# Performance work log

Hardware: AMD Instinct MI355X
Metric: run time of the kernel (lower is better)

The kernel has to match this reference:

```python
import jax, jax.numpy as jnp
import numpy as np

D = 4096  # uniform layer width (sizes[i])
L = 4     # number of MyLinear layers (maximum)


def setup_inputs() -> dict:
    key = jax.random.key(0)
    ks = jax.random.split(key, 8)
    x = jax.random.normal(ks[0], (D,), jnp.float32)
    W_in = jax.random.normal(ks[1], (D, D), jnp.float32) / np.float32(np.sqrt(D))
    b_in = jax.random.normal(ks[2], (D,), jnp.float32) * 0.01
    weights = jax.random.normal(ks[3], (L, D, D), jnp.float32) / np.float32(np.sqrt(D))
    # `order` is a fixed 0/1-style connectivity mask (requires_grad=False in torch)
    orders = (jax.random.uniform(ks[4], (L, D, D)) < 0.5).astype(jnp.float32)
    biases = jax.random.normal(ks[5], (L, D), jnp.float32) * 0.01
    # input_layer[i]: which node slots feed layer i (irregular gather)
    gather_idx = jax.random.randint(ks[6], (L, D), 0, D)
    # layer_nodes[k]: where layer outputs are scattered (per-layer permutation)
    scatter_idx = jnp.stack(
        [jax.random.permutation(jax.random.fold_in(ks[7], i), D) for i in range(L + 1)]
    )
    return dict(x=x, W_in=W_in, b_in=b_in, weights=weights, orders=orders,
                biases=biases, gather_idx=gather_idx, scatter_idx=scatter_idx)


def reference(x, W_in, b_in, weights, orders, biases, gather_idx, scatter_idx):
    # input layer: relu(Linear(x)), scattered into the node buffer
    out0 = jax.nn.relu(W_in @ x + b_in)              # [D]
    buf = jnp.zeros_like(out0).at[scatter_idx[0]].set(out0)

    def step(buf, layer):
        W, O, b, g, s = layer
        inp = buf[g]                                  # gather node values [D]
        out = jax.nn.relu((W * O) @ inp + b)          # masked GEMV + bias + relu
        new_buf = jnp.zeros_like(out).at[s].set(out)  # scatter into node buffer
        return new_buf, out

    _, outs = jax.lax.scan(
        step, buf, (weights, orders, biases, gather_idx, scatter_idx[1:])
    )
    return outs[-1]  # forward returns the last layer's (pre-scatter) output
```

## Files before the change

kernel.cpp:

```cpp
#include <hip/hip_runtime.h>
#include <hip/hip_bf16.h>


#define DD 4096
#define NB 256
#define NT 1024
#define NLAYER 4

__device__ __forceinline__ void grid_barrier(int* cnt) {
    __syncthreads();
    if (threadIdx.x == 0) {
        __threadfence();
        __hip_atomic_fetch_add(cnt, 1, __ATOMIC_ACQ_REL, __HIP_MEMORY_SCOPE_AGENT);
        while (__hip_atomic_load(cnt, __ATOMIC_ACQUIRE, __HIP_MEMORY_SCOPE_AGENT) < NB) {}
        __threadfence();
    }
    __syncthreads();
}

__global__ __launch_bounds__(NT, 4)
void fused_net(const float* __restrict__ x,
               const float* __restrict__ W_in,
               const float* __restrict__ b_in,
               const float* __restrict__ weights,
               const float* __restrict__ orders,
               const float* __restrict__ biases,
               const int*   __restrict__ gidx,
               const int*   __restrict__ sidx,
               float*       __restrict__ out,
               float*       __restrict__ buf0,
               float*       __restrict__ buf1,
               int*         __restrict__ cnt)
{
    __shared__ float sh[DD];
    const int tid  = threadIdx.x;
    const int lane = tid & 63;
    const int wv   = tid >> 6;
    const int row  = blockIdx.x * 16 + wv;

    for (int j = tid; j < DD; j += NT) sh[j] = x[j];
    __syncthreads();
    {
        const float* Wr = W_in + (size_t)row * DD + lane * 4;
        float a0 = 0.f, a1 = 0.f, a2 = 0.f, a3 = 0.f;
        #pragma unroll
        for (int it = 0; it < 16; ++it) {
            float4 w = *reinterpret_cast<const float4*>(Wr + it * 256);
            float4 v = *reinterpret_cast<const float4*>(sh + it * 256 + lane * 4);
            a0 = fmaf(w.x, v.x, a0); a1 = fmaf(w.y, v.y, a1);
            a2 = fmaf(w.z, v.z, a2); a3 = fmaf(w.w, v.w, a3);
        }
        float acc = (a0 + a1) + (a2 + a3);
        #pragma unroll
        for (int off = 32; off; off >>= 1) acc += __shfl_xor(acc, off, 64);
        if (lane == 0) buf0[sidx[row]] = fmaxf(acc + b_in[row], 0.f);
    }
    grid_barrier(cnt + 0);

    float* bufs[2] = { buf0, buf1 };
    #pragma unroll
    for (int l = 0; l < NLAYER; ++l) {
        const float* src = bufs[l & 1];
        const int*   g   = gidx + (size_t)l * DD;
        for (int j = tid; j < DD; j += NT) sh[j] = src[g[j]];
        __syncthreads();

        const float* Wr = weights + (size_t)l * DD * DD + (size_t)row * DD + lane * 4;
        const float* Or = orders  + (size_t)l * DD * DD + (size_t)row * DD + lane * 4;
        float a0 = 0.f, a1 = 0.f, a2 = 0.f, a3 = 0.f;
        #pragma unroll
        for (int it = 0; it < 16; ++it) {
            float4 w = *reinterpret_cast<const float4*>(Wr + it * 256);
            float4 o = *reinterpret_cast<const float4*>(Or + it * 256);
            float4 v = *reinterpret_cast<const float4*>(sh + it * 256 + lane * 4);
            a0 = fmaf(w.x * o.x, v.x, a0);
            a1 = fmaf(w.y * o.y, v.y, a1);
            a2 = fmaf(w.z * o.z, v.z, a2);
            a3 = fmaf(w.w * o.w, v.w, a3);
        }
        float acc = (a0 + a1) + (a2 + a3);
        #pragma unroll
        for (int off = 32; off; off >>= 1) acc += __shfl_xor(acc, off, 64);
        float r = fmaxf(acc + biases[(size_t)l * DD + row], 0.f);

        if (l == NLAYER - 1) {
            if (lane == 0) out[row] = r;
        } else {
            if (lane == 0) bufs[(l + 1) & 1][sidx[(size_t)(l + 1) * DD + row]] = r;
            grid_barrier(cnt + 1 + l);
        }
    }
}

extern "C" void kernel_launch(void* const* d_in, const int* in_sizes, int n_in,
                              void* d_out, int out_size, void* d_ws, size_t ws_size,
                              hipStream_t stream) {
    const float* x       = (const float*)d_in[0];
    const float* W_in    = (const float*)d_in[1];
    const float* b_in    = (const float*)d_in[2];
    const float* weights = (const float*)d_in[3];
    const float* orders  = (const float*)d_in[4];
    const float* biases  = (const float*)d_in[5];
    const int*   gidx    = (const int*)d_in[6];
    const int*   sidx    = (const int*)d_in[7];
    float*       out     = (float*)d_out;

    int*   cnt  = (int*)d_ws;
    float* buf0 = (float*)((char*)d_ws + 256);
    float* buf1 = buf0 + DD;

    hipMemsetAsync(d_ws, 0, 256, stream);

    fused_net<<<NB, NT, 0, stream>>>(x, W_in, b_in, weights, orders, biases,
                                     gidx, sidx, out, buf0, buf1, cnt);
}
```

Baseline: 660.4 us.

## Split each row across two waves and double the grid to 512 blocks

Each block now handles 8 rows, with two wavefronts each computing half of a row's dot product. The halves are combined through shared memory, so the grid doubles to 512 blocks and launch bounds rise to 8. The inner loop software-prefetches the next weight and mask float4, and the barrier spin adds s_sleep to reduce atomic polling pressure. The aim is more memory-level parallelism across CUs for this bandwidth-bound masked GEMV. The cost is an extra shared-memory reduction and more blocks arriving at each grid barrier, and the persistent-grid scheme now relies on all 512 blocks being co-resident.

```diff
diff --git a/kernel.cpp b/kernel.cpp
--- a/kernel.cpp
+++ b/kernel.cpp
@@ -3,22 +3,58 @@
 
 
 #define DD 4096
-#define NB 256
+#define NB 512
 #define NT 1024
 #define NLAYER 4
+#define ROWS_PER_BLOCK 8
 
 __device__ __forceinline__ void grid_barrier(int* cnt) {
     __syncthreads();
     if (threadIdx.x == 0) {
         __threadfence();
         __hip_atomic_fetch_add(cnt, 1, __ATOMIC_ACQ_REL, __HIP_MEMORY_SCOPE_AGENT);
-        while (__hip_atomic_load(cnt, __ATOMIC_ACQUIRE, __HIP_MEMORY_SCOPE_AGENT) < NB) {}
+        while (__hip_atomic_load(cnt, __ATOMIC_ACQUIRE, __HIP_MEMORY_SCOPE_AGENT) < NB)
+            __builtin_amdgcn_s_sleep(2);
         __threadfence();
     }
     __syncthreads();
 }
 
-__global__ __launch_bounds__(NT, 4)
+template<bool MASKED>
+__device__ __forceinline__ float half_row_dot(const float* __restrict__ Wr,
+                                              const float* __restrict__ Or,
+                                              const float* __restrict__ sh,
+                                              int half, int lane)
+{
+    const int base = half * 2048 + lane * 4;
+    float4 w0 = *reinterpret_cast<const float4*>(Wr + base);
+    float4 o0;
+    if (MASKED) o0 = *reinterpret_cast<const float4*>(Or + base);
+
+    float a0 = 0.f, a1 = 0.f, a2 = 0.f, a3 = 0.f;
+    #pragma unroll
+    for (int it = 0; it < 8; ++it) {
+        float4 wn, on;
+        if (it < 7) {
+            wn = *reinterpret_cast<const float4*>(Wr + base + (it + 1) * 256);
+            if (MASKED) on = *reinterpret_cast<const float4*>(Or + base + (it + 1) * 256);
+        }
+        float4 v = *reinterpret_cast<const float4*>(sh + base + it * 256);
+        if (MASKED) { w0.x *= o0.x; w0.y *= o0.y; w0.z *= o0.z; w0.w *= o0.w; }
+        a0 = fmaf(w0.x, v.x, a0);
+        a1 = fmaf(w0.y, v.y, a1);
+        a2 = fmaf(w0.z, v.z, a2);
+        a3 = fmaf(w0.w, v.w, a3);
+        w0 = wn;
+        if (MASKED) o0 = on;
+    }
+    float acc = (a0 + a1) + (a2 + a3);
+    #pragma unroll
+    for (int off = 32; off; off >>= 1) acc += __shfl_xor(acc, off, 64);
+    return acc;
+}
+
+__global__ __launch_bounds__(NT, 8)
 void fused_net(const float* __restrict__ x,
                const float* __restrict__ W_in,
                const float* __restrict__ b_in,
@@ -33,27 +69,26 @@
                int*         __restrict__ cnt)
 {
     __shared__ float sh[DD];
+    __shared__ float partial[16];
     const int tid  = threadIdx.x;
     const int lane = tid & 63;
     const int wv   = tid >> 6;
-    const int row  = blockIdx.x * 16 + wv;
+    const int rl   = wv >> 1;
+    const int half = wv & 1;
+    const int row  = blockIdx.x * ROWS_PER_BLOCK + rl;
 
     for (int j = tid; j < DD; j += NT) sh[j] = x[j];
     __syncthreads();
     {
-        const float* Wr = W_in + (size_t)row * DD + lane * 4;
-        float a0 = 0.f, a1 = 0.f, a2 = 0.f, a3 = 0.f;
-        #pragma unroll
-        for (int it = 0; it < 16; ++it) {
-            float4 w = *reinterpret_cast<const float4*>(Wr + it * 256);
-            float4 v = *reinterpret_cast<const float4*>(sh + it * 256 + lane * 4);
-            a0 = fmaf(w.x, v.x, a0); a1 = fmaf(w.y, v.y, a1);
-            a2 = fmaf(w.z, v.z, a2); a3 = fmaf(w.w, v.w, a3);
-        }
-        float acc = (a0 + a1) + (a2 + a3);
-        #pragma unroll
-        for (int off = 32; off; off >>= 1) acc += __shfl_xor(acc, off, 64);
-        if (lane == 0) buf0[sidx[row]] = fmaxf(acc + b_in[row], 0.f);
+        const float* Wr = W_in + (size_t)row * DD;
+        float acc = half_row_dot<false>(Wr, nullptr, sh, half, lane);
+        if (lane == 0) partial[wv] = acc;
+    }
+    __syncthreads();
+    if (tid < ROWS_PER_BLOCK) {
+        const int r = blockIdx.x * ROWS_PER_BLOCK + tid;
+        float v = partial[2 * tid] + partial[2 * tid + 1] + b_in[r];
+        buf0[sidx[r]] = fmaxf(v, 0.f);
     }
     grid_barrier(cnt + 0);
 
@@ -65,30 +100,22 @@
         for (int j = tid; j < DD; j += NT) sh[j] = src[g[j]];
         __syncthreads();
 
-        const float* Wr = weights + (size_t)l * DD * DD + (size_t)row * DD + lane * 4;
-        const float* Or = orders  + (size_t)l * DD * DD + (size_t)row * DD + lane * 4;
-        float a0 = 0.f, a1 = 0.f, a2 = 0.f, a3 = 0.f;
-        #pragma unroll
-        for (int it = 0; it < 16; ++it) {
-            float4 w = *reinterpret_cast<const float4*>(Wr + it * 256);
-            float4 o = *reinterpret_cast<const float4*>(Or + it * 256);
-            float4 v = *reinterpret_cast<const float4*>(sh + it * 256 + lane * 4);
-            a0 = fmaf(w.x * o.x, v.x, a0);
-            a1 = fmaf(w.y * o.y, v.y, a1);
-            a2 = fmaf(w.z * o.z, v.z, a2);
-            a3 = fmaf(w.w * o.w, v.w, a3);
+        const float* Wr = weights + (size_t)l * DD * DD + (size_t)row * DD;
+        const float* Or = orders  + (size_t)l * DD * DD + (size_t)row * DD;
+        float acc = half_row_dot<true>(Wr, Or, sh, half, lane);
+        if (lane == 0) partial[wv] = acc;
+        __syncthreads();
+
+        if (tid < ROWS_PER_BLOCK) {
+            const int r = blockIdx.x * ROWS_PER_BLOCK + tid;
+            float v = partial[2 * tid] + partial[2 * tid + 1]
+                    + biases[(size_t)l * DD + r];
+            v = fmaxf(v, 0.f);
+            if (l == NLAYER - 1) out[r] = v;
+            else bufs[(l + 1) & 1][sidx[(size_t)(l + 1) * DD + r]] = v;
         }
-        float acc = (a0 + a1) + (a2 + a3);
-        #pragma unroll
-        for (int off = 32; off; off >>= 1) acc += __shfl_xor(acc, off, 64);
-        float r = fmaxf(acc + biases[(size_t)l * DD + row], 0.f);
-
-        if (l == NLAYER - 1) {
-            if (lane == 0) out[row] = r;
-        } else {
-            if (lane == 0) bufs[(l + 1) & 1][sidx[(size_t)(l + 1) * DD + row]] = r;
-            grid_barrier(cnt + 1 + l);
-        }
+        if (l < NLAYER - 1) grid_barrier(cnt + 1 + l);
+        else __syncthreads();
     }
 }
 
```

Measured after the change: 900.9 us. 1.36x slower.
